# Optimization experiments

Hardware: AMD Instinct MI355X
Metric: run time of the kernel (lower is better)

The kernel has to match this reference:

```python
import jax, jax.numpy as jnp
import numpy as np

SR = 44100
WT_LEN = 512
N_WT = 20
B, T = 16, 262144


def setup_inputs() -> dict:
    key = jax.random.key(0)
    k1, k2, k3, k4 = jax.random.split(key, 4)
    # realistic fundamental frequencies in [50, 500) Hz
    pitch = 50.0 + 450.0 * jax.random.uniform(k1, (B, T, 1), dtype=jnp.float32)
    amplitude = jax.random.uniform(k2, (B, T, 1), dtype=jnp.float32)
    attention = jax.random.uniform(k3, (B, T, N_WT), dtype=jnp.float32)
    # learned wavetables [N_WT, WT_LEN]; first 4 are fixed sine cycles, rest learnable noise
    i = np.arange(WT_LEN, dtype=np.float32)
    sines = np.stack([np.sin((c + 1) * 2 * np.pi * i / WT_LEN) for c in range(4)]).astype(np.float32)
    rest = 0.01 * np.asarray(jax.random.normal(k4, (N_WT - 4, WT_LEN)), dtype=np.float32)
    wt = np.concatenate([sines, rest], axis=0)
    # module enforces wt[-1] == wt[0] (periodic closure)
    wt[:, -1] = wt[:, 0]
    return {"pitch": pitch, "amplitude": amplitude, "attention": attention,
            "wavetables": jnp.asarray(wt)}


def reference(pitch, amplitude, attention, wavetables):
    L = wavetables.shape[1]
    # tanh applied to learnable tables only (indices >= 4)
    wt = jnp.concatenate([wavetables[:4], jnp.tanh(wavetables[4:])], axis=0)  # [K, L]
    freq = pitch[..., 0]                                   # [B, T]
    increment = freq / SR * L                              # [B, T]
    index = jnp.cumsum(increment, axis=-1) - increment[:, :1]
    index = index % L
    idx_low = jnp.floor(index)
    idx_high = jnp.ceil(index)
    alpha = index - idx_low                                # [B, T]
    il = idx_low.astype(jnp.int32)
    ih = (idx_high.astype(jnp.int32)) % L
    wt_t = wt.T                                            # [L, K]
    low = wt_t[il]                                         # [B, T, K] single gather for all tables
    high = wt_t[ih]                                        # [B, T, K]
    waveforms = low + alpha[..., None] * (high - low)      # [B, T, K]
    mixed = jnp.sum(waveforms * attention, axis=-1)        # [B, T]
    return (mixed[..., None] * amplitude)                  # [B, T, 1]
```

## Files before the change

### kernel.cpp

```cpp
#include <hip/hip_runtime.h>
#include <math.h>

#define WT_LEN 512
#define N_WT 20
#define B_ 16
#define T_ 262144
#define TOTAL (B_ * T_)
#define CHUNK 8192
#define NCHR 32
#define NCH  512

__device__ __forceinline__ float to_inc1(float x) {
    return (x / 44100.0f) * 512.0f;
}
__device__ __forceinline__ float4 to_inc4(float4 p) {
    float4 r;
    r.x = to_inc1(p.x); r.y = to_inc1(p.y);
    r.z = to_inc1(p.z); r.w = to_inc1(p.w);
    return r;
}

__global__ __launch_bounds__(1024) void up_kernel(
        const float* __restrict__ pitch, float* __restrict__ A13) {
    __shared__ float red[2048];
    const int t = threadIdx.x;
    const size_t g0 = (size_t)blockIdx.x * CHUNK;

    const float4* p4 = (const float4*)(pitch + g0);
    float4 v0 = to_inc4(p4[2 * t]);
    float4 v1 = to_inc4(p4[2 * t + 1]);
    float t0 = v0.x + v0.y, t1 = v0.z + v0.w;
    float t2 = v1.x + v1.y, t3 = v1.z + v1.w;
    red[t] = (t0 + t1) + (t2 + t3);
    __syncthreads();
    int off_prev = 0, off = 1024;
    for (int sz = 512; sz >= 1; sz >>= 1) {
        if (t < sz) red[off + t] = red[off_prev + 2 * t] + red[off_prev + 2 * t + 1];
        __syncthreads();
        off_prev = off; off += sz;
    }
    if (t == 0) A13[blockIdx.x] = red[2046];
}

__global__ __launch_bounds__(1024) void mid_kernel(
        const float* __restrict__ A13, const float* __restrict__ pitch,
        const float* __restrict__ wtg, float* __restrict__ S13,
        float* __restrict__ X0, float* __restrict__ WTT) {
    int r = threadIdx.x;
    if (r < B_) {
        float l0[32], l1[16], l2[8], l3[4], l4[2], l5;
        for (int i = 0; i < 32; ++i) l0[i] = A13[r * 32 + i];
        for (int i = 0; i < 16; ++i) l1[i] = l0[2 * i] + l0[2 * i + 1];
        for (int i = 0; i < 8;  ++i) l2[i] = l1[2 * i] + l1[2 * i + 1];
        for (int i = 0; i < 4;  ++i) l3[i] = l2[2 * i] + l2[2 * i + 1];
        for (int i = 0; i < 2;  ++i) l4[i] = l3[2 * i] + l3[2 * i + 1];
        l5 = l4[0] + l4[1];

        float s4[2], s3[4], s2[8], s1[16], s0[32];
        s4[0] = l4[0]; s4[1] = l5;
        s3[0] = l3[0];
        for (int i = 0; i < 2; ++i) {
            s3[2 * i + 1] = s4[i];
            if (2 * i + 2 < 4) s3[2 * i + 2] = s4[i] + l3[2 * i + 2];
        }
        s2[0] = l2[0];
        for (int i = 0; i < 4; ++i) {
            s2[2 * i + 1] = s3[i];
            if (2 * i + 2 < 8) s2[2 * i + 2] = s3[i] + l2[2 * i + 2];
        }
        s1[0] = l1[0];
        for (int i = 0; i < 8; ++i) {
            s1[2 * i + 1] = s2[i];
            if (2 * i + 2 < 16) s1[2 * i + 2] = s2[i] + l1[2 * i + 2];
        }
        s0[0] = l0[0];
        for (int i = 0; i < 16; ++i) {
            s0[2 * i + 1] = s1[i];
            if (2 * i + 2 < 32) s0[2 * i + 2] = s1[i] + l0[2 * i + 2];
        }
        for (int i = 0; i < 32; ++i) S13[r * 32 + i] = s0[i];
        X0[r] = to_inc1(pitch[(size_t)r * T_]);
    }
    for (int e = threadIdx.x; e < WT_LEN * N_WT; e += 1024) {
        int c = e / WT_LEN;
        int i = e - c * WT_LEN;
        float v = wtg[e];
        if (c >= 4) v = tanhf(v);
        WTT[i * N_WT + c] = v;
    }
}

__global__ __launch_bounds__(1024) void down_kernel(
        const float* __restrict__ pitch, const float* __restrict__ S13,
        float* __restrict__ sout) {
    __shared__ float a[2048];
    const int t = threadIdx.x;
    const int c = blockIdx.x;
    const size_t g0 = (size_t)c * CHUNK;

    const float4* p4 = (const float4*)(pitch + g0);
    float4 va = to_inc4(p4[2 * t]);
    float4 vb = to_inc4(p4[2 * t + 1]);
    float x0 = va.x, x2 = va.z, x4 = vb.x, x6 = vb.z;
    float t0 = va.x + va.y, t1 = va.z + va.w;
    float t2 = vb.x + vb.y, t3 = vb.z + vb.w;
    float u0 = t0 + t1, u1 = t2 + t3;
    a[t] = u0 + u1;
    __syncthreads();

    int bp = 0, b = 1024;
    for (int sz = 512; sz >= 2; sz >>= 1) {
        if (t < sz) a[b + t] = a[bp + 2 * t] + a[bp + 2 * t + 1];
        __syncthreads();
        bp = b; b += sz;
    }

    const float P   = (c & (NCHR - 1)) ? S13[c - 1] : 0.0f;
    const float T13 = S13[c];
    if (t == 0) {
        a[2044] = P + a[2044];
        a[2045] = T13;
    }
    __syncthreads();

    const int offk[10] = {0, 1024, 1536, 1792, 1920, 1984, 2016, 2032, 2040, 2044};
    for (int k = 11; k >= 3; --k) {
        int m = 1 << (13 - k), half = m >> 1;
        int bk = offk[k - 3], bn = offk[k - 2];
        if (t < half) {
            float sn = a[bn + t];
            int j = 2 * t + 2;
            float av = (j < m) ? a[bk + j] : 0.0f;
            a[bk + 2 * t + 1] = sn;
            if (j < m) a[bk + j] = sn + av;
        }
        if (t == 0) a[bk] = P + a[bk];
        __syncthreads();
    }

    float S3prev = t ? a[t - 1] : P;
    float s3t = a[t];
    float s1a = S3prev + t0;
    float s2a = S3prev + u0;
    float s1c = s2a + t2;
    (void)t1; (void)t3; (void)u1;

    float4* q4 = (float4*)(sout + g0);
    q4[2 * t]     = make_float4(S3prev + x0, s1a, s1a + x2, s2a);
    q4[2 * t + 1] = make_float4(s2a + x4, s1c, s1c + x6, s3t);
}

__global__ __launch_bounds__(512) void mix_kernel(
        float* io, const float* __restrict__ X0,
        const float* __restrict__ amp, const float* __restrict__ att,
        const float* __restrict__ WTT, int ntiles) {
    __shared__ float wt_lds[WT_LEN * N_WT];
    {
        const float4* src = (const float4*)WTT;
        float4* dst = (float4*)wt_lds;
#pragma unroll
        for (int r = 0; r < 5; ++r)
            dst[threadIdx.x + 512 * r] = src[threadIdx.x + 512 * r];
    }
    __syncthreads();

    for (int tile = blockIdx.x; tile < ntiles; tile += gridDim.x) {
        int gid = tile * 512 + threadIdx.x;
        int row = gid >> 18;
        float S = io[gid];
        float y = S - X0[row];

        float qf  = floorf(y * (1.0f / 512.0f));
        float idx = fmaf(-512.0f, qf, y);
        if (idx < 0.0f)    idx += 512.0f;
        if (idx >= 512.0f) idx -= 512.0f;

        float fl0   = floorf(idx);
        float alpha = idx - fl0;
        int il = ((int)fl0) & (WT_LEN - 1);
        int ih = (il + (alpha > 0.0f ? 1 : 0)) & (WT_LEN - 1);

        const float4* lo4 = (const float4*)(&wt_lds[il * N_WT]);
        const float4* hi4 = (const float4*)(&wt_lds[ih * N_WT]);
        const float4* a4  = (const float4*)(att + (size_t)gid * N_WT);

        float acc = 0.0f;
#pragma unroll
        for (int v = 0; v < 5; ++v) {
            float4 lo = lo4[v];
            float4 hi = hi4[v];
            float4 at = a4[v];
            acc += at.x * (lo.x + alpha * (hi.x - lo.x));
            acc += at.y * (lo.y + alpha * (hi.y - lo.y));
            acc += at.z * (lo.z + alpha * (hi.z - lo.z));
            acc += at.w * (lo.w + alpha * (hi.w - lo.w));
        }
        io[gid] = acc * amp[gid];
    }
}

extern "C" void kernel_launch(void* const* d_in, const int* in_sizes, int n_in,
                              void* d_out, int out_size, void* d_ws, size_t ws_size,
                              hipStream_t stream) {
    const float* pitch = (const float*)d_in[0];
    const float* amp   = (const float*)d_in[1];
    const float* att   = (const float*)d_in[2];
    const float* wtg   = (const float*)d_in[3];
    float* S = (float*)d_out;

    float* A13 = (float*)d_ws;
    float* S13 = A13 + NCH;
    float* X0  = S13 + NCH;
    float* WTT = X0 + 64;

    up_kernel<<<NCH, 1024, 0, stream>>>(pitch, A13);
    mid_kernel<<<1, 1024, 0, stream>>>(A13, pitch, wtg, S13, X0, WTT);
    down_kernel<<<NCH, 1024, 0, stream>>>(pitch, S13, S);
    mix_kernel<<<1024, 512, 0, stream>>>(S, X0, amp, att, WTT,
                                         TOTAL / 512);
}
```

Baseline: 501.3 us.

## Fuse scan down-sweep with wavetable mixing to skip phase buffer round trip

```diff
diff --git a/kernel.cpp b/kernel.cpp
--- a/kernel.cpp
+++ b/kernel.cpp
@@ -90,10 +90,12 @@
     }
 }
 
-__global__ __launch_bounds__(1024) void down_kernel(
+__global__ __launch_bounds__(1024) void downmix_kernel(
         const float* __restrict__ pitch, const float* __restrict__ S13,
-        float* __restrict__ sout) {
-    __shared__ float a[2048];
+        const float* __restrict__ X0,    const float* __restrict__ amp,
+        const float* __restrict__ att,   const float* __restrict__ WTT,
+        float* __restrict__ out) {
+    __shared__ float lds[WT_LEN * N_WT];
     const int t = threadIdx.x;
     const int c = blockIdx.x;
     const size_t g0 = (size_t)c * CHUNK;
@@ -105,12 +107,12 @@
     float t0 = va.x + va.y, t1 = va.z + va.w;
     float t2 = vb.x + vb.y, t3 = vb.z + vb.w;
     float u0 = t0 + t1, u1 = t2 + t3;
-    a[t] = u0 + u1;
+    lds[t] = u0 + u1;
     __syncthreads();
 
     int bp = 0, b = 1024;
     for (int sz = 512; sz >= 2; sz >>= 1) {
-        if (t < sz) a[b + t] = a[bp + 2 * t] + a[bp + 2 * t + 1];
+        if (t < sz) lds[b + t] = lds[bp + 2 * t] + lds[bp + 2 * t + 1];
         __syncthreads();
         bp = b; b += sz;
     }
@@ -118,8 +120,8 @@
     const float P   = (c & (NCHR - 1)) ? S13[c - 1] : 0.0f;
     const float T13 = S13[c];
     if (t == 0) {
-        a[2044] = P + a[2044];
-        a[2045] = T13;
+        lds[2044] = P + lds[2044];
+        lds[2045] = T13;
     }
     __syncthreads();
 
@@ -128,47 +130,47 @@
         int m = 1 << (13 - k), half = m >> 1;
         int bk = offk[k - 3], bn = offk[k - 2];
         if (t < half) {
-            float sn = a[bn + t];
+            float sn = lds[bn + t];
             int j = 2 * t + 2;
-            float av = (j < m) ? a[bk + j] : 0.0f;
-            a[bk + 2 * t + 1] = sn;
-            if (j < m) a[bk + j] = sn + av;
-        }
-        if (t == 0) a[bk] = P + a[bk];
+            float av = (j < m) ? lds[bk + j] : 0.0f;
+            lds[bk + 2 * t + 1] = sn;
+            if (j < m) lds[bk + j] = sn + av;
+        }
+        if (t == 0) lds[bk] = P + lds[bk];
         __syncthreads();
     }
 
-    float S3prev = t ? a[t - 1] : P;
-    float s3t = a[t];
-    float s1a = S3prev + t0;
-    float s2a = S3prev + u0;
-    float s1c = s2a + t2;
+    float S3prev = t ? lds[t - 1] : P;
+    float s3t = lds[t];
+    float s[8];
+    s[0] = S3prev + x0;
+    s[1] = S3prev + t0;
+    s[2] = s[1] + x2;
+    s[3] = S3prev + u0;
+    s[4] = s[3] + x4;
+    s[5] = s[3] + t2;
+    s[6] = s[5] + x6;
+    s[7] = s3t;
     (void)t1; (void)t3; (void)u1;
-
-    float4* q4 = (float4*)(sout + g0);
-    q4[2 * t]     = make_float4(S3prev + x0, s1a, s1a + x2, s2a);
-    q4[2 * t + 1] = make_float4(s2a + x4, s1c, s1c + x6, s3t);
-}
-
-__global__ __launch_bounds__(512) void mix_kernel(
-        float* io, const float* __restrict__ X0,
-        const float* __restrict__ amp, const float* __restrict__ att,
-        const float* __restrict__ WTT, int ntiles) {
-    __shared__ float wt_lds[WT_LEN * N_WT];
+    __syncthreads();
+
     {
         const float4* src = (const float4*)WTT;
-        float4* dst = (float4*)wt_lds;
+        float4* dst = (float4*)lds;
+        for (int e = t; e < (WT_LEN * N_WT) / 4; e += 1024) dst[e] = src[e];
+    }
+    __syncthreads();
+
+    const float x0r = X0[c >> 5];
+    const size_t e0 = g0 + (size_t)t * 8;
+    float4 am0 = ((const float4*)(amp + e0))[0];
+    float4 am1 = ((const float4*)(amp + e0))[1];
+    float amv[8] = {am0.x, am0.y, am0.z, am0.w, am1.x, am1.y, am1.z, am1.w};
+    float o[8];
+
 #pragma unroll
-        for (int r = 0; r < 5; ++r)
-            dst[threadIdx.x + 512 * r] = src[threadIdx.x + 512 * r];
-    }
-    __syncthreads();
-
-    for (int tile = blockIdx.x; tile < ntiles; tile += gridDim.x) {
-        int gid = tile * 512 + threadIdx.x;
-        int row = gid >> 18;
-        float S = io[gid];
-        float y = S - X0[row];
+    for (int j = 0; j < 8; ++j) {
+        float y = s[j] - x0r;
 
         float qf  = floorf(y * (1.0f / 512.0f));
         float idx = fmaf(-512.0f, qf, y);
@@ -180,9 +182,9 @@
         int il = ((int)fl0) & (WT_LEN - 1);
         int ih = (il + (alpha > 0.0f ? 1 : 0)) & (WT_LEN - 1);
 
-        const float4* lo4 = (const float4*)(&wt_lds[il * N_WT]);
-        const float4* hi4 = (const float4*)(&wt_lds[ih * N_WT]);
-        const float4* a4  = (const float4*)(att + (size_t)gid * N_WT);
+        const float4* lo4 = (const float4*)(&lds[il * N_WT]);
+        const float4* hi4 = (const float4*)(&lds[ih * N_WT]);
+        const float4* a4  = (const float4*)(att + (e0 + j) * N_WT);
 
         float acc = 0.0f;
 #pragma unroll
@@ -195,8 +197,12 @@
             acc += at.z * (lo.z + alpha * (hi.z - lo.z));
             acc += at.w * (lo.w + alpha * (hi.w - lo.w));
         }
-        io[gid] = acc * amp[gid];
-    }
+        o[j] = acc * amv[j];
+    }
+
+    float4* q4 = (float4*)(out + e0);
+    q4[0] = make_float4(o[0], o[1], o[2], o[3]);
+    q4[1] = make_float4(o[4], o[5], o[6], o[7]);
 }
 
 extern "C" void kernel_launch(void* const* d_in, const int* in_sizes, int n_in,
@@ -206,7 +212,7 @@
     const float* amp   = (const float*)d_in[1];
     const float* att   = (const float*)d_in[2];
     const float* wtg   = (const float*)d_in[3];
-    float* S = (float*)d_out;
+    float* out = (float*)d_out;
 
     float* A13 = (float*)d_ws;
     float* S13 = A13 + NCH;
@@ -215,7 +221,6 @@
 
     up_kernel<<<NCH, 1024, 0, stream>>>(pitch, A13);
     mid_kernel<<<1, 1024, 0, stream>>>(A13, pitch, wtg, S13, X0, WTT);
-    down_kernel<<<NCH, 1024, 0, stream>>>(pitch, S13, S);
-    mix_kernel<<<1024, 512, 0, stream>>>(S, X0, amp, att, WTT,
-                                         TOTAL / 512);
-}
+    downmix_kernel<<<NCH, 1024, 0, stream>>>(pitch, S13, X0, amp, att, WTT,
+                                             out);
+}
```

New measurement: 545.4 us. +8.8%, slower.
